# Performance work log

Measured on AMD Instinct MI355X. Metric: run time of the kernel, lower is better.

The kernel has to match this reference:

```python
import jax, jax.numpy as jnp
import numpy as np

POS_THR = 0.5
NEG_THR = 0.4
WEIGHTS = (1.0, 1.0, 1.0, 1.0)


def _box_iou(a, b):
    # a: (N,4), b: (M,4) in xyxy -> (N,M) IoU
    area_a = (a[:, 2] - a[:, 0]) * (a[:, 3] - a[:, 1])  # (N,)
    area_b = (b[:, 2] - b[:, 0]) * (b[:, 3] - b[:, 1])  # (M,)
    lt = jnp.maximum(a[:, None, :2], b[None, :, :2])  # (N,M,2)
    rb = jnp.minimum(a[:, None, 2:], b[None, :, 2:])  # (N,M,2)
    wh = jnp.clip(rb - lt, 0.0)
    inter = wh[..., 0] * wh[..., 1]  # (N,M)
    return inter / (area_a[:, None] + area_b[None, :] - inter)


def _encode(anchors, gt):
    # both (N,4) xyxy -> (N,4) deltas (dx,dy,dw,dh)
    eps = jnp.finfo(jnp.float32).eps
    ax = (anchors[:, 0] + anchors[:, 2]) * 0.5
    ay = (anchors[:, 1] + anchors[:, 3]) * 0.5
    aw = jnp.maximum(anchors[:, 2] - anchors[:, 0], eps)
    ah = jnp.maximum(anchors[:, 3] - anchors[:, 1], eps)
    gx = (gt[:, 0] + gt[:, 2]) * 0.5
    gy = (gt[:, 1] + gt[:, 3]) * 0.5
    gw = gt[:, 2] - gt[:, 0]
    gh = gt[:, 3] - gt[:, 1]
    dx = (gx - ax) / aw
    dy = (gy - ay) / ah
    dw = jnp.log(gw / aw)
    dh = jnp.log(gh / ah)
    w = jnp.asarray(WEIGHTS, dtype=jnp.float32)
    return jnp.stack((dx, dy, dw, dh), axis=-1) * w


def setup_inputs() -> dict:
    key = jax.random.key(0)
    k1, k2, k3, k4, k5 = jax.random.split(key, 5)
    N, M, IMG = 200000, 128, 1024.0
    # valid anchor boxes: random centers + sizes in [8, 512]
    ac = jax.random.uniform(k1, (N, 2), dtype=jnp.float32) * IMG
    asz = 8.0 + jax.random.uniform(k2, (N, 2), dtype=jnp.float32) * 504.0
    anchors = jnp.concatenate([ac - 0.5 * asz, ac + 0.5 * asz], axis=-1)
    gc = jax.random.uniform(k3, (M, 2), dtype=jnp.float32) * IMG
    gsz = 16.0 + jax.random.uniform(k4, (M, 2), dtype=jnp.float32) * 480.0
    gt_boxes = jnp.concatenate([gc - 0.5 * gsz, gc + 0.5 * gsz], axis=-1)
    gt_labels = jax.random.randint(k5, (M,), 1, 81, dtype=jnp.int64 if jax.config.jax_enable_x64 else jnp.int32)
    return {"anchors": anchors, "gt_boxes": gt_boxes, "gt_labels": gt_labels}


def reference(anchors, gt_boxes, gt_labels):
    iou = _box_iou(anchors, gt_boxes)  # (N,M)
    max_iou_per_anchor = iou.max(axis=1)              # (N,)
    matched_gt_idx = iou.argmax(axis=1)               # (N,)
    matched_anchor_per_gt = iou.argmax(axis=0)        # (M,)
    pos_mask = max_iou_per_anchor >= POS_THR
    pos_mask = pos_mask.at[matched_anchor_per_gt].set(True)  # force best anchor per gt positive
    neg_mask = (max_iou_per_anchor < NEG_THR) & (~pos_mask)
    cls_targets = jnp.where(pos_mask, gt_labels[matched_gt_idx].astype(jnp.int32),
                            jnp.where(neg_mask, 0, -1))
    enc = _encode(anchors, gt_boxes[matched_gt_idx])  # (N,4)
    reg_targets = jnp.where(pos_mask[:, None], enc, 0.0)
    return cls_targets, reg_targets, pos_mask
```

## Files before the change

kernel.cpp:

```cpp
#include <hip/hip_runtime.h>
#include <cmath>
#include <cstdint>

typedef unsigned long long ull;

constexpr float POS_THR = 0.5f;
constexpr float NEG_THR = 0.4f;
constexpr float F32_EPS = 1.1920928955078125e-07f;

__device__ __forceinline__ float iou_one(const float4 a, const float area_a,
                                         const float4 g, const float area_g) {
    float lx = fmaxf(a.x, g.x);
    float ly = fmaxf(a.y, g.y);
    float rx = fminf(a.z, g.z);
    float ry = fminf(a.w, g.w);
    float w  = fmaxf(rx - lx, 0.0f);
    float h  = fmaxf(ry - ly, 0.0f);
    float inter = w * h;
    return inter / (area_a + area_g - inter);
}

__device__ __forceinline__ float4 encode_box(const float4 a, const float4 g) {
    float ax = (a.x + a.z) * 0.5f;
    float ay = (a.y + a.w) * 0.5f;
    float aw = fmaxf(a.z - a.x, F32_EPS);
    float ah = fmaxf(a.w - a.y, F32_EPS);
    float gx = (g.x + g.z) * 0.5f;
    float gy = (g.y + g.w) * 0.5f;
    float gw = g.z - g.x;
    float gh = g.w - g.y;
    return make_float4((gx - ax) / aw, (gy - ay) / ah, logf(gw / aw), logf(gh / ah));
}

__device__ __forceinline__ ull shfl_xor_u64(ull key, int off) {
    unsigned lo = (unsigned)key;
    unsigned hi = (unsigned)(key >> 32);
    lo = __shfl_xor(lo, off, 64);
    hi = __shfl_xor(hi, off, 64);
    return ((ull)hi << 32) | lo;
}

__device__ __forceinline__ ull pack_key(float v, unsigned idx) {
    return ((ull)__float_as_uint(v) << 32) | (ull)(~idx);
}

__global__ __launch_bounds__(256, 4) void fused_kernel(
    const float4* __restrict__ anchors, const float4* __restrict__ gts,
    const int* __restrict__ labels, int n, int m, int nblocks,
    float* __restrict__ out_cls, float4* __restrict__ out_reg,
    float* __restrict__ out_pos, ull* __restrict__ ws)
{
    __shared__ float4 sA[128];
    __shared__ float  sAa[128];
    __shared__ float4 sG[128];
    __shared__ float  sLab[128];
    __shared__ ull    sK[128][17];

    const int t = threadIdx.x;
    const int base = blockIdx.x * 128;

    if (t < 128) {
        int i = base + t;
        float4 a = make_float4(0.0f, 0.0f, 0.0f, 0.0f);
        if (i < n) a = anchors[i];
        sA[t]  = a;
        sAa[t] = (a.z - a.x) * (a.w - a.y);
    } else {
        int j = t - 128;
        sG[j] = gts[j];
        sLab[j] = (float)labels[j];
    }

    const int tx = t & 15;
    const int ty = t >> 4;
    const int g0 = tx * 8;
    const int a0 = ty * 8;

    float4 g[8];
    float  ga[8];
    #pragma unroll
    for (int j = 0; j < 8; ++j) {
        g[j]  = gts[g0 + j];
        ga[j] = (g[j].z - g[j].x) * (g[j].w - g[j].y);
    }

    float cbest[8];
    int   cbi[8];
    #pragma unroll
    for (int j = 0; j < 8; ++j) { cbest[j] = -1.0f; cbi[j] = 0; }

    __syncthreads();

    #pragma unroll
    for (int ap = 0; ap < 4; ++ap) {
        const int ai0 = 2 * ap, ai1 = 2 * ap + 1;
        float4 aA = sA[a0 + ai0];  float aaA = sAa[a0 + ai0];
        float4 aB = sA[a0 + ai1];  float aaB = sAa[a0 + ai1];
        float rbA = -1.0f, rbB = -1.0f;
        int   rjA = 0,     rjB = 0;
        #pragma unroll
        for (int j = 0; j < 8; ++j) {
            float v0 = iou_one(aA, aaA, g[j], ga[j]);
            float v1 = iou_one(aB, aaB, g[j], ga[j]);
            if (v0 > rbA) { rbA = v0; rjA = j; }
            if (v1 > rbB) { rbB = v1; rjB = j; }
            float vm = fmaxf(v0, v1);
            int   am = (v0 >= v1) ? ai0 : ai1;
            if (vm > cbest[j]) { cbest[j] = vm; cbi[j] = am; }
        }
        sK[a0 + ai0][tx] = pack_key(rbA, (unsigned)(g0 + rjA));
        sK[a0 + ai1][tx] = pack_key(rbB, (unsigned)(g0 + rjB));
    }
    __syncthreads();

    if (t < 128) {
        ull k = sK[t][0];
        #pragma unroll
        for (int x = 1; x < 16; ++x) { ull o = sK[t][x]; if (o > k) k = o; }
        int i = base + t;
        if (i < n) {
            float best = __uint_as_float((unsigned)(k >> 32));
            int bestj  = (int)(~(unsigned)k);
            bool pos = best >= POS_THR;
            bool neg = (best < NEG_THR) && !pos;
            out_cls[i] = pos ? sLab[bestj] : (neg ? 0.0f : -1.0f);
            out_pos[i] = pos ? 1.0f : 0.0f;
            float4 enc = make_float4(0.0f, 0.0f, 0.0f, 0.0f);
            if (pos) enc = encode_box(sA[t], sG[bestj]);
            out_reg[i] = enc;
        }
    }
    __syncthreads();

    #pragma unroll
    for (int j = 0; j < 8; ++j) {
        sK[g0 + j][ty] = pack_key(cbest[j], (unsigned)(base + a0 + cbi[j]));
    }
    __syncthreads();

    if (t < 128) {
        ull k = sK[t][0];
        #pragma unroll
        for (int y = 1; y < 16; ++y) { ull o = sK[t][y]; if (o > k) k = o; }
        ws[(size_t)t * nblocks + blockIdx.x] = k;
    }
}

__global__ __launch_bounds__(256) void reduce_fixup(
    const float4* __restrict__ anchors, const float4* __restrict__ gts,
    const int* __restrict__ labels, int n, int m, int nblocks,
    float* __restrict__ out_cls, float4* __restrict__ out_reg,
    float* __restrict__ out_pos, const ull* __restrict__ ws)
{
    __shared__ ull wk[4];
    __shared__ ull s_winner;
    const int j = blockIdx.x;
    const int t = threadIdx.x;
    const ull* wj = ws + (size_t)j * nblocks;

    ull key = 0ull;
    for (int b = t; b < nblocks; b += 256) {
        ull k = wj[b];
        if (k > key) key = k;
    }
    #pragma unroll
    for (int off = 32; off > 0; off >>= 1) {
        ull o = shfl_xor_u64(key, off);
        if (o > key) key = o;
    }
    if ((t & 63) == 0) wk[t >> 6] = key;
    __syncthreads();
    if (t == 0) {
        ull k = wk[0];
        #pragma unroll
        for (int w = 1; w < 4; ++w) if (wk[w] > k) k = wk[w];
        s_winner = k;
    }
    __syncthreads();
    const unsigned gi = ~(unsigned)(s_winner & 0xFFFFFFFFull);

    if (t < 64) {
        float4 a = anchors[gi];
        float area_a = (a.z - a.x) * (a.w - a.y);
        ull k2 = 0ull;
        for (int jj = t; jj < m; jj += 64) {
            float4 g = gts[jj];
            float area_g = (g.z - g.x) * (g.w - g.y);
            float v = iou_one(a, area_a, g, area_g);
            ull kk = ((ull)__float_as_uint(v) << 32) | (ull)(~(unsigned)jj);
            if (kk > k2) k2 = kk;
        }
        #pragma unroll
        for (int off = 32; off > 0; off >>= 1) {
            ull o = shfl_xor_u64(k2, off);
            if (o > k2) k2 = o;
        }
        if (t == 0) {
            int bj = (int)(~(unsigned)(k2 & 0xFFFFFFFFull));
            out_pos[gi] = 1.0f;
            out_cls[gi] = (float)labels[bj];
            out_reg[gi] = encode_box(a, gts[bj]);
        }
    }
}

extern "C" void kernel_launch(void* const* d_in, const int* in_sizes, int n_in,
                              void* d_out, int out_size, void* d_ws, size_t ws_size,
                              hipStream_t stream)
{
    const float4* anchors = (const float4*)d_in[0];
    const float4* gts     = (const float4*)d_in[1];
    const int*    labels  = (const int*)d_in[2];
    int n = in_sizes[0] / 4;
    int m = in_sizes[1] / 4;

    float*  out     = (float*)d_out;
    float*  out_cls = out;
    float4* out_reg = (float4*)(out + n);
    float*  out_pos = out + 5 * (size_t)n;
    ull*    ws      = (ull*)d_ws;

    int nblocks = (n + 127) / 128;
    fused_kernel<<<nblocks, 256, 0, stream>>>(anchors, gts, labels, n, m, nblocks,
                                              out_cls, out_reg, out_pos, ws);
    reduce_fixup<<<m, 256, 0, stream>>>(anchors, gts, labels, n, m, nblocks,
                                        out_cls, out_reg, out_pos, ws);
}
```

Before: 91.05 us.

## Drop per-gt anchor index tracking; recover winner anchor in fixup kernel

The main kernel no longer tracks the argmax anchor index per gt column. It keeps only the column max value and records the winning block index in the workspace key. The fixup kernel recomputes IoU over the 128 anchors of the winning block to find the exact anchor, then finds its best gt. It also turns off FP contraction and uses explicitly rounded arithmetic so the recomputed IoUs match bit for bit, and splits the row keys into 32-bit value and index arrays in shared memory. The aim is less register pressure and fewer selects in the hot inner loop, at the cost of extra work in the fixup and possibly slower non-fused arithmetic.

```diff
diff --git a/kernel.cpp b/kernel.cpp
--- a/kernel.cpp
+++ b/kernel.cpp
@@ -2,11 +2,17 @@
 #include <cmath>
 #include <cstdint>
 
+#pragma clang fp contract(off)
+
 typedef unsigned long long ull;
 
 constexpr float POS_THR = 0.5f;
 constexpr float NEG_THR = 0.4f;
 constexpr float F32_EPS = 1.1920928955078125e-07f;
+
+__device__ __forceinline__ float area_of(const float4 b) {
+    return __fmul_rn(__fsub_rn(b.z, b.x), __fsub_rn(b.w, b.y));
+}
 
 __device__ __forceinline__ float iou_one(const float4 a, const float area_a,
                                          const float4 g, const float area_g) {
@@ -14,10 +20,11 @@
     float ly = fmaxf(a.y, g.y);
     float rx = fminf(a.z, g.z);
     float ry = fminf(a.w, g.w);
-    float w  = fmaxf(rx - lx, 0.0f);
-    float h  = fmaxf(ry - ly, 0.0f);
-    float inter = w * h;
-    return inter / (area_a + area_g - inter);
+    float w  = fmaxf(__fsub_rn(rx, lx), 0.0f);
+    float h  = fmaxf(__fsub_rn(ry, ly), 0.0f);
+    float inter = __fmul_rn(w, h);
+    float denom = __fsub_rn(__fadd_rn(area_a, area_g), inter);
+    return __fdiv_rn(inter, denom);
 }
 
 __device__ __forceinline__ float4 encode_box(const float4 a, const float4 g) {
@@ -40,21 +47,15 @@
     return ((ull)hi << 32) | lo;
 }
 
-__device__ __forceinline__ ull pack_key(float v, unsigned idx) {
-    return ((ull)__float_as_uint(v) << 32) | (ull)(~idx);
-}
-
 __global__ __launch_bounds__(256, 4) void fused_kernel(
     const float4* __restrict__ anchors, const float4* __restrict__ gts,
     const int* __restrict__ labels, int n, int m, int nblocks,
     float* __restrict__ out_cls, float4* __restrict__ out_reg,
     float* __restrict__ out_pos, ull* __restrict__ ws)
 {
-    __shared__ float4 sA[128];
-    __shared__ float  sAa[128];
-    __shared__ float4 sG[128];
-    __shared__ float  sLab[128];
-    __shared__ ull    sK[128][17];
+    __shared__ float4   sA[128];
+    __shared__ unsigned sKv[128][17];
+    __shared__ unsigned sKi[128][17];
 
     const int t = threadIdx.x;
     const int base = blockIdx.x * 128;
@@ -63,12 +64,7 @@
         int i = base + t;
         float4 a = make_float4(0.0f, 0.0f, 0.0f, 0.0f);
         if (i < n) a = anchors[i];
-        sA[t]  = a;
-        sAa[t] = (a.z - a.x) * (a.w - a.y);
-    } else {
-        int j = t - 128;
-        sG[j] = gts[j];
-        sLab[j] = (float)labels[j];
+        sA[t] = a;
     }
 
     const int tx = t & 15;
@@ -81,21 +77,22 @@
     #pragma unroll
     for (int j = 0; j < 8; ++j) {
         g[j]  = gts[g0 + j];
-        ga[j] = (g[j].z - g[j].x) * (g[j].w - g[j].y);
+        ga[j] = area_of(g[j]);
     }
 
     float cbest[8];
-    int   cbi[8];
-    #pragma unroll
-    for (int j = 0; j < 8; ++j) { cbest[j] = -1.0f; cbi[j] = 0; }
+    #pragma unroll
+    for (int j = 0; j < 8; ++j) cbest[j] = -1.0f;
 
     __syncthreads();
 
     #pragma unroll
     for (int ap = 0; ap < 4; ++ap) {
         const int ai0 = 2 * ap, ai1 = 2 * ap + 1;
-        float4 aA = sA[a0 + ai0];  float aaA = sAa[a0 + ai0];
-        float4 aB = sA[a0 + ai1];  float aaB = sAa[a0 + ai1];
+        float4 aA = sA[a0 + ai0];
+        float4 aB = sA[a0 + ai1];
+        float aaA = area_of(aA);
+        float aaB = area_of(aB);
         float rbA = -1.0f, rbB = -1.0f;
         int   rjA = 0,     rjB = 0;
         #pragma unroll
@@ -104,103 +101,125 @@
             float v1 = iou_one(aB, aaB, g[j], ga[j]);
             if (v0 > rbA) { rbA = v0; rjA = j; }
             if (v1 > rbB) { rbB = v1; rjB = j; }
-            float vm = fmaxf(v0, v1);
-            int   am = (v0 >= v1) ? ai0 : ai1;
-            if (vm > cbest[j]) { cbest[j] = vm; cbi[j] = am; }
-        }
-        sK[a0 + ai0][tx] = pack_key(rbA, (unsigned)(g0 + rjA));
-        sK[a0 + ai1][tx] = pack_key(rbB, (unsigned)(g0 + rjB));
+            cbest[j] = fmaxf(cbest[j], fmaxf(v0, v1));
+        }
+        sKv[a0 + ai0][tx] = __float_as_uint(rbA);
+        sKi[a0 + ai0][tx] = ~(unsigned)(g0 + rjA);
+        sKv[a0 + ai1][tx] = __float_as_uint(rbB);
+        sKi[a0 + ai1][tx] = ~(unsigned)(g0 + rjB);
     }
     __syncthreads();
 
     if (t < 128) {
-        ull k = sK[t][0];
-        #pragma unroll
-        for (int x = 1; x < 16; ++x) { ull o = sK[t][x]; if (o > k) k = o; }
+        unsigned bv = sKv[t][0];
+        unsigned bi = sKi[t][0];
+        #pragma unroll
+        for (int x = 1; x < 16; ++x) {
+            unsigned v = sKv[t][x], i2 = sKi[t][x];
+            if (v > bv || (v == bv && i2 > bi)) { bv = v; bi = i2; }
+        }
         int i = base + t;
         if (i < n) {
-            float best = __uint_as_float((unsigned)(k >> 32));
-            int bestj  = (int)(~(unsigned)k);
+            float best = __uint_as_float(bv);
+            int bestj  = (int)(~bi);
             bool pos = best >= POS_THR;
             bool neg = (best < NEG_THR) && !pos;
-            out_cls[i] = pos ? sLab[bestj] : (neg ? 0.0f : -1.0f);
+            out_cls[i] = pos ? (float)labels[bestj] : (neg ? 0.0f : -1.0f);
             out_pos[i] = pos ? 1.0f : 0.0f;
             float4 enc = make_float4(0.0f, 0.0f, 0.0f, 0.0f);
-            if (pos) enc = encode_box(sA[t], sG[bestj]);
+            if (pos) enc = encode_box(sA[t], gts[bestj]);
             out_reg[i] = enc;
         }
     }
     __syncthreads();
 
     #pragma unroll
-    for (int j = 0; j < 8; ++j) {
-        sK[g0 + j][ty] = pack_key(cbest[j], (unsigned)(base + a0 + cbi[j]));
-    }
+    for (int j = 0; j < 8; ++j)
+        sKv[g0 + j][ty] = __float_as_uint(cbest[j]);
     __syncthreads();
 
     if (t < 128) {
-        ull k = sK[t][0];
-        #pragma unroll
-        for (int y = 1; y < 16; ++y) { ull o = sK[t][y]; if (o > k) k = o; }
-        ws[(size_t)t * nblocks + blockIdx.x] = k;
-    }
-}
-
-__global__ __launch_bounds__(256) void reduce_fixup(
+        unsigned bv = sKv[t][0];
+        #pragma unroll
+        for (int y = 1; y < 16; ++y) { unsigned v = sKv[t][y]; if (v > bv) bv = v; }
+        ws[(size_t)t * nblocks + blockIdx.x] =
+            ((ull)bv << 32) | (ull)(~(unsigned)blockIdx.x);
+    }
+}
+
+__global__ __launch_bounds__(128) void reduce_fixup(
     const float4* __restrict__ anchors, const float4* __restrict__ gts,
     const int* __restrict__ labels, int n, int m, int nblocks,
     float* __restrict__ out_cls, float4* __restrict__ out_reg,
     float* __restrict__ out_pos, const ull* __restrict__ ws)
 {
-    __shared__ ull wk[4];
-    __shared__ ull s_winner;
+    __shared__ ull redu[2];
+    __shared__ ull s_akey;
+    __shared__ ull s_bkey;
+    __shared__ ull s_ckey;
+
     const int j = blockIdx.x;
     const int t = threadIdx.x;
     const ull* wj = ws + (size_t)j * nblocks;
 
     ull key = 0ull;
-    for (int b = t; b < nblocks; b += 256) {
-        ull k = wj[b];
-        if (k > key) key = k;
-    }
+    for (int b = t; b < nblocks; b += 128) { ull k = wj[b]; if (k > key) key = k; }
     #pragma unroll
     for (int off = 32; off > 0; off >>= 1) {
         ull o = shfl_xor_u64(key, off);
         if (o > key) key = o;
     }
-    if ((t & 63) == 0) wk[t >> 6] = key;
+    if ((t & 63) == 0) redu[t >> 6] = key;
+    __syncthreads();
+    if (t == 0) s_akey = redu[0] > redu[1] ? redu[0] : redu[1];
+    __syncthreads();
+    const unsigned B = ~(unsigned)s_akey;
+
+    float4 gj = gts[j];
+    float gaj = area_of(gj);
+    {
+        int i = (int)B * 128 + t;
+        float4 a = make_float4(0.0f, 0.0f, 0.0f, 0.0f);
+        if (i < n) a = anchors[i];
+        float aa = area_of(a);
+        float v = iou_one(a, aa, gj, gaj);
+        ull kb = ((ull)__float_as_uint(v) << 32) | (ull)(~(unsigned)t);
+        #pragma unroll
+        for (int off = 32; off > 0; off >>= 1) {
+            ull o = shfl_xor_u64(kb, off);
+            if (o > kb) kb = o;
+        }
+        __syncthreads();
+        if ((t & 63) == 0) redu[t >> 6] = kb;
+    }
+    __syncthreads();
+    if (t == 0) s_bkey = redu[0] > redu[1] ? redu[0] : redu[1];
+    __syncthreads();
+    const int giW = (int)B * 128 + (int)(~(unsigned)s_bkey);
+
+    float4 aw = anchors[giW];
+    float aaw = area_of(aw);
+    ull k2 = 0ull;
+    if (t < m) {
+        float4 gt_t = gts[t];
+        float gat = area_of(gt_t);
+        float v2 = iou_one(aw, aaw, gt_t, gat);
+        k2 = ((ull)__float_as_uint(v2) << 32) | (ull)(~(unsigned)t);
+    }
+    #pragma unroll
+    for (int off = 32; off > 0; off >>= 1) {
+        ull o = shfl_xor_u64(k2, off);
+        if (o > k2) k2 = o;
+    }
+    __syncthreads();
+    if ((t & 63) == 0) redu[t >> 6] = k2;
     __syncthreads();
     if (t == 0) {
-        ull k = wk[0];
-        #pragma unroll
-        for (int w = 1; w < 4; ++w) if (wk[w] > k) k = wk[w];
-        s_winner = k;
-    }
-    __syncthreads();
-    const unsigned gi = ~(unsigned)(s_winner & 0xFFFFFFFFull);
-
-    if (t < 64) {
-        float4 a = anchors[gi];
-        float area_a = (a.z - a.x) * (a.w - a.y);
-        ull k2 = 0ull;
-        for (int jj = t; jj < m; jj += 64) {
-            float4 g = gts[jj];
-            float area_g = (g.z - g.x) * (g.w - g.y);
-            float v = iou_one(a, area_a, g, area_g);
-            ull kk = ((ull)__float_as_uint(v) << 32) | (ull)(~(unsigned)jj);
-            if (kk > k2) k2 = kk;
-        }
-        #pragma unroll
-        for (int off = 32; off > 0; off >>= 1) {
-            ull o = shfl_xor_u64(k2, off);
-            if (o > k2) k2 = o;
-        }
-        if (t == 0) {
-            int bj = (int)(~(unsigned)(k2 & 0xFFFFFFFFull));
-            out_pos[gi] = 1.0f;
-            out_cls[gi] = (float)labels[bj];
-            out_reg[gi] = encode_box(a, gts[bj]);
-        }
+        s_ckey = redu[0] > redu[1] ? redu[0] : redu[1];
+        int bj = (int)(~(unsigned)s_ckey);
+        out_pos[giW] = 1.0f;
+        out_cls[giW] = (float)labels[bj];
+        out_reg[giW] = encode_box(aw, gts[bj]);
     }
 }
 
@@ -223,6 +242,6 @@
     int nblocks = (n + 127) / 128;
     fused_kernel<<<nblocks, 256, 0, stream>>>(anchors, gts, labels, n, m, nblocks,
                                               out_cls, out_reg, out_pos, ws);
-    reduce_fixup<<<m, 256, 0, stream>>>(anchors, gts, labels, n, m, nblocks,
+    reduce_fixup<<<m, 128, 0, stream>>>(anchors, gts, labels, n, m, nblocks,
                                         out_cls, out_reg, out_pos, ws);
 }
```

Result: slower. 93.23 us (+2.4%).
